# Kernel optimization log

Measured on AMD Instinct MI355X. Metric: run time of the kernel, lower is better.

## Reference

```python
import jax, jax.numpy as jnp
import numpy as np

CHUNK = 64
EPS = 1e-5


def segsum(a):
    # a: (..., T) -> (..., T, T) lower-triangular cumulative segment sums; -inf above diag
    T = a.shape[-1]
    cs = jnp.cumsum(a, axis=-1)
    ss = cs[..., :, None] - cs[..., None, :]
    mask = jnp.tril(jnp.ones((T, T), dtype=bool))
    return jnp.where(mask, ss, -jnp.inf)


def ssd(x, A, B, C, chunk):
    # x: (b, L, h, p), A: (b, L, h), B/C: (b, L, n)
    b, L, h, p = x.shape
    c = L // chunk
    x = x.reshape(b, c, chunk, h, p)
    A = A.reshape(b, c, chunk, h).transpose(0, 3, 1, 2)          # b h c l
    B = B.reshape(b, c, chunk, -1)                               # b c l n
    C = C.reshape(b, c, chunk, -1)                               # b c l n
    A_cum = jnp.cumsum(A, axis=-1)                               # b h c l
    Lmat = jnp.exp(segsum(A))                                    # b h c l l (causal decay)
    # intra-chunk (diagonal-block) output
    Y_diag = jnp.einsum('bcln,bcsn,bhcls,bcshp->bclhp', C, B, Lmat, x)
    # per-chunk states
    decay_states = jnp.exp(A_cum[..., -1:] - A_cum)              # b h c l
    states = jnp.einsum('bcln,bhcl,bclhp->bchpn', B, decay_states, x)
    states = jnp.concatenate([jnp.zeros_like(states[:, :1]), states], axis=1)  # b (c+1) h p n
    # inter-chunk recurrence via chunk-level segsum
    A_last = jnp.pad(A_cum[..., -1], ((0, 0), (0, 0), (1, 0)))   # b h (c+1)
    decay_chunk = jnp.exp(segsum(A_last))                        # b h (c+1) (c+1)
    new_states = jnp.einsum('bhzc,bchpn->bzhpn', decay_chunk, states)
    states, final = new_states[:, :-1], new_states[:, -1:]
    Y_off = jnp.einsum('bcln,bchpn,bhcl->bclhp', C, states, jnp.exp(A_cum))
    return (Y_diag + Y_off).reshape(b, L, h, p), final


def mamba2(x, W_in, conv_w, conv_b, dt_bias, A_log, D, norm_w, W_out):
    d_inner = norm_w.shape[0]
    nheads = dt_bias.shape[0]
    d_state = (conv_b.shape[0] - d_inner) // 2
    headdim = d_inner // nheads
    k_conv = conv_w.shape[0]
    b, L, _ = x.shape

    zxbcdt = x @ W_in                                            # (b, L, 2*d_inner+2*n+h)
    z = zxbcdt[..., :d_inner]
    xBC = zxbcdt[..., d_inner:2 * d_inner + 2 * d_state]
    dt = jax.nn.softplus(zxbcdt[..., 2 * d_inner + 2 * d_state:] + dt_bias)  # (b, L, h)
    A = -jnp.exp(A_log)                                          # (h,)

    # causal depthwise conv (zero init conv state == left-pad k_conv-1 zeros) + silu
    xp = jnp.pad(xBC, ((0, 0), (k_conv - 1, 0), (0, 0)))
    xBC = jax.lax.conv_general_dilated(
        xp, conv_w, (1,), 'VALID',
        dimension_numbers=('NWC', 'WIO', 'NWC'),
        feature_group_count=conv_b.shape[0])
    xBC = jax.nn.silu(xBC + conv_b)

    xs = xBC[..., :d_inner].reshape(b, L, nheads, headdim)       # (b, L, h, p)
    Bm = xBC[..., d_inner:d_inner + d_state]                     # (b, L, n)
    Cm = xBC[..., d_inner + d_state:]                            # (b, L, n)

    Y, _ = ssd(xs * dt[..., None], A * dt, Bm, Cm, CHUNK)
    Y = Y + xs * D                                               # D: (h, 1) broadcasts over p
    y = Y.reshape(b, L, d_inner)

    # gated RMSNorm
    y = y * jax.nn.silu(z)
    y = y * jax.lax.rsqrt(jnp.mean(y * y, axis=-1, keepdims=True) + EPS) * norm_w
    return y @ W_out


def setup_inputs():
    key = jax.random.key(0)
    ks = jax.random.split(key, 8)
    B, L, d_model = 2, 4096, 1024
    expand, d_state, k_conv, headdim = 2, 128, 4, 64
    d_inner = expand * d_model
    nheads = d_inner // headdim
    d_in_proj = 2 * d_inner + 2 * d_state + nheads
    conv_dim = d_inner + 2 * d_state
    return {
        'x': jax.random.normal(ks[0], (B, L, d_model), jnp.float32),
        'W_in': jax.random.normal(ks[1], (d_model, d_in_proj), jnp.float32) / np.sqrt(d_model).astype(np.float32),
        'conv_w': jax.random.normal(ks[2], (k_conv, 1, conv_dim), jnp.float32) / np.sqrt(k_conv).astype(np.float32),
        'conv_b': jnp.zeros((conv_dim,), jnp.float32),
        'dt_bias': jax.random.normal(ks[3], (nheads,), jnp.float32) * 0.5 - 2.0,
        'A_log': jnp.log(1.0 + 15.0 * jax.random.uniform(ks[4], (nheads,), jnp.float32)),
        'D': jax.random.normal(ks[5], (nheads, 1), jnp.float32),
        'norm_w': jnp.ones((d_inner,), jnp.float32),
        'W_out': jax.random.normal(ks[6], (d_inner, d_model), jnp.float32) / np.sqrt(d_inner).astype(np.float32),
    }


def reference(x, W_in, conv_w, conv_b, dt_bias, A_log, D, norm_w, W_out):
    return mamba2(x, W_in, conv_w, conv_b, dt_bias, A_log, D, norm_w, W_out)
```

## Files before the change

### kernel.cpp

```cpp
#include <hip/hip_runtime.h>
#include <hip/hip_fp16.h>

typedef _Float16 f16;
typedef _Float16 f16x4 __attribute__((ext_vector_type(4)));
typedef _Float16 f16x8 __attribute__((ext_vector_type(8)));
typedef float f32x4 __attribute__((ext_vector_type(4)));

#define DEV __device__ __forceinline__

constexpr int BB    = 2;
constexpr int LL    = 4096;
constexpr int DM    = 1024;
constexpr int DIN   = 2048;
constexpr int DST   = 128;
constexpr int NH    = 32;
constexpr int HD    = 64;
constexpr int NC    = 64;
constexpr int MROWS = BB * LL;
constexpr int NPROJ = 2*DIN + 2*DST + NH;
constexpr int NZ    = 2*DIN + 2*DST;
constexpr int CONVD = DIN + 2*DST;
constexpr int DT_OFF = 2*DIN + 2*DST;
constexpr int BOFF  = DIN;
constexpr int COFF  = DIN + DST;

DEV float silu_f(float v) { return v / (1.f + __expf(-v)); }

DEV void gload_lds16(const f16* gsrc, f16* lds_dst) {
  __builtin_amdgcn_global_load_lds(
      (const __attribute__((address_space(1))) void*)gsrc,
      (__attribute__((address_space(3))) void*)lds_dst, 16, 0, 0);
}

__global__ __launch_bounds__(256)
void tof16_kernel(const float* __restrict__ src, f16* __restrict__ dst, int n8) {
  int i = blockIdx.x * 256 + threadIdx.x;
  if (i >= n8) return;
  f32x4 a = *(const f32x4*)(src + (size_t)i*8);
  f32x4 b = *(const f32x4*)(src + (size_t)i*8 + 4);
  f16x8 o;
#pragma unroll
  for (int j = 0; j < 4; ++j) { o[j] = (f16)a[j]; o[4+j] = (f16)b[j]; }
  *(f16x8*)(dst + (size_t)i*8) = o;
}

__global__ __launch_bounds__(256)
void transpose_f32_to_f16(const float* __restrict__ src, f16* __restrict__ dst,
                          int K, int N, int srcLd, const float* __restrict__ colScale) {
  __shared__ float tbuf[32][33];
  int n0 = blockIdx.x * 32, k0 = blockIdx.y * 32;
  int tx = threadIdx.x & 31, ty = threadIdx.x >> 5;
  for (int i = ty; i < 32; i += 8)
    tbuf[i][tx] = src[(size_t)(k0 + i)*srcLd + n0 + tx];
  __syncthreads();
  float cs = colScale ? colScale[k0 + tx] : 1.f;
  for (int i = ty; i < 32; i += 8)
    dst[(size_t)(n0 + i)*K + (k0 + tx)] = (f16)(tbuf[tx][i] * cs);
}

template<int BM, int BN, int WM_, int WN_, bool C16>
__global__ __launch_bounds__(WM_*WN_*64, 2)
void gemm_t(const f16* __restrict__ A, const f16* __restrict__ Bt,
            void* __restrict__ Cp, int M, int N, int K, int ldc,
            const float* __restrict__ rowScale) {
  constexpr int THREADS = WM_*WN_*64;
  constexpr int WTM = BM/WM_, WTN = BN/WN_;
  constexpr int FM = WTM/16, FN = WTN/16;
  constexpr int LA = BM*4/THREADS, LB = BN*4/THREADS;
  __shared__ f16 As[2][BM*32];
  __shared__ f16 Bs[2][BN*32];
  const int nbn = N / BN;
  const int nwg = (int)gridDim.x;
  const int lb  = ((int)blockIdx.x & 7) * (nwg >> 3) + ((int)blockIdx.x >> 3);
  const int bm = lb / nbn, bn = lb % nbn;
  const int tid = threadIdx.x;
  const int wave = tid >> 6, lane = tid & 63;
  const int lrow = lane & 15, kgrp = lane >> 4;
  const int wm = wave / WN_, wn = wave % WN_;
  const int nt = K >> 5;
  const int bcol8 = (kgrp ^ ((lrow ^ (lrow >> 2)) & 3)) * 8;

  const f16* aptr[LA];
  const f16* bptr[LB];
#pragma unroll
  for (int i = 0; i < LA; ++i) {
    int s = tid + i*THREADS, row = s >> 2;
    int g = (s & 3) ^ ((row ^ (row >> 2)) & 3);
    aptr[i] = A + (size_t)(bm*BM + row)*K + g*8;
  }
#pragma unroll
  for (int i = 0; i < LB; ++i) {
    int s = tid + i*THREADS, row = s >> 2;
    int g = (s & 3) ^ ((row ^ (row >> 2)) & 3);
    bptr[i] = Bt + (size_t)(bn*BN + row)*K + g*8;
  }

  f32x4 acc[FM][FN] = {};

  auto STAGE = [&](int buf, int t) {
#pragma unroll
    for (int i = 0; i < LA; ++i)
      gload_lds16(aptr[i] + (size_t)t*32, As[buf] + (wave*64 + i*THREADS)*8);
#pragma unroll
    for (int i = 0; i < LB; ++i)
      gload_lds16(bptr[i] + (size_t)t*32, Bs[buf] + (wave*64 + i*THREADS)*8);
  };

  STAGE(0, 0);
  asm volatile("s_waitcnt vmcnt(0)" ::: "memory");
  __builtin_amdgcn_s_barrier();
  __builtin_amdgcn_sched_barrier(0);

  for (int t = 0; t < nt; ++t) {
    const int cur = t & 1;
    if (t + 1 < nt) STAGE(cur ^ 1, t + 1);
    const f16* Ab = As[cur];
    const f16* Bb = Bs[cur];
    f16x8 bf[FN];
#pragma unroll
    for (int n = 0; n < FN; ++n)
      bf[n] = *(const f16x8*)(Bb + (wn*WTN + n*16 + lrow)*32 + bcol8);
#pragma unroll
    for (int m = 0; m < FM; ++m) {
      f16x8 af = *(const f16x8*)(Ab + (wm*WTM + m*16 + lrow)*32 + bcol8);
#pragma unroll
      for (int n = 0; n < FN; ++n)
        acc[m][n] = __builtin_amdgcn_mfma_f32_16x16x32_f16(af, bf[n], acc[m][n], 0, 0, 0);
    }
    if (t + 1 < nt) {
      asm volatile("s_waitcnt vmcnt(0)" ::: "memory");
      __builtin_amdgcn_s_barrier();
      __builtin_amdgcn_sched_barrier(0);
    }
  }

  int crow0 = bm*BM + wm*WTM, ccol0 = bn*BN + wn*WTN;
#pragma unroll
  for (int m = 0; m < FM; ++m)
#pragma unroll
    for (int n = 0; n < FN; ++n) {
      int r0 = crow0 + m*16 + (lane >> 4)*4;
      int c0 = ccol0 + n*16 + (lane & 15);
#pragma unroll
      for (int r = 0; r < 4; ++r) {
        float v = acc[m][n][r];
        if (rowScale) v *= rowScale[r0 + r];
        if constexpr (C16) {
          f16* C = (f16*)Cp;
          C[(size_t)(r0 + r)*ldc + c0] = (f16)v;
        } else {
          float* C = (float*)Cp;
          C[(size_t)(r0 + r)*ldc + c0] = v;
        }
      }
    }
}

__global__ __launch_bounds__(256)
void dt_kernel(const float* __restrict__ x, const float* __restrict__ Win,
               const float* __restrict__ dt_bias, const float* __restrict__ A_log,
               float* __restrict__ dt, float* __restrict__ Acum) {
  __shared__ float xs[64][132];
  __shared__ float ws[128][32];
  __shared__ float dts[64][32];
  int bc = blockIdx.x;
  int r0 = bc * 64;
  int t = threadIdx.x;
  int r = t >> 2, c0 = (t & 3) * 8;
  float acc[8] = {};
  for (int kt = 0; kt < 1024; kt += 128) {
    __syncthreads();
#pragma unroll
    for (int i = 0; i < 8; ++i) {
      int idx4 = t + i*256;
      int rr = idx4 >> 5, c4 = (idx4 & 31) * 4;
      *(f32x4*)&xs[rr][c4] = *(const f32x4*)(x + (size_t)(r0 + rr)*1024 + kt + c4);
    }
#pragma unroll
    for (int i = 0; i < 4; ++i) {
      int idx4 = t + i*256;
      int rr = idx4 >> 3, c4 = (idx4 & 7) * 4;
      *(f32x4*)&ws[rr][c4] = *(const f32x4*)(Win + (size_t)(kt + rr)*NPROJ + DT_OFF + c4);
    }
    __syncthreads();
#pragma unroll 8
    for (int k = 0; k < 128; ++k) {
      float xv = xs[r][k];
      f32x4 w0 = *(const f32x4*)&ws[k][c0];
      f32x4 w1 = *(const f32x4*)&ws[k][c0 + 4];
#pragma unroll
      for (int j = 0; j < 4; ++j) { acc[j] += xv * w0[j]; acc[4+j] += xv * w1[j]; }
    }
  }
#pragma unroll
  for (int j = 0; j < 8; ++j) {
    float v = acc[j] + dt_bias[c0 + j];
    float sp = (v > 20.f) ? v : log1pf(__expf(v));
    dt[(size_t)(r0 + r)*NH + c0 + j] = sp;
    dts[r][c0 + j] = sp;
  }
  __syncthreads();
  int wave = t >> 6, lane = t & 63;
  for (int hh = 0; hh < 8; ++hh) {
    int h = wave*8 + hh;
    float A = -__expf(A_log[h]);
    float v = A * dts[lane][h];
#pragma unroll
    for (int off = 1; off < 64; off <<= 1) {
      float u = __shfl_up(v, off);
      if (lane >= off) v += u;
    }
    Acum[((size_t)bc*NH + h)*64 + lane] = v;
  }
}

__global__ __launch_bounds__(256)
void conv_kernel(const f16* __restrict__ zxh, const float* __restrict__ cw,
                 const float* __restrict__ cb, f16* __restrict__ out) {
  int i = blockIdx.x * 256 + threadIdx.x;
  int row = i / (CONVD/8);
  int c8  = (i - row*(CONVD/8)) * 8;
  int lb = row & (LL - 1);
  f32x4 a0 = *(const f32x4*)(cb + c8);
  f32x4 a1 = *(const f32x4*)(cb + c8 + 4);
#pragma unroll
  for (int j = 0; j < 4; ++j) {
    int lsrc = lb - 3 + j;
    if (lsrc >= 0) {
      f16x8 v = *(const f16x8*)(zxh + (size_t)(row - 3 + j)*NZ + BOFF + c8);
      f32x4 w0 = *(const f32x4*)(cw + j*CONVD + c8);
      f32x4 w1 = *(const f32x4*)(cw + j*CONVD + c8 + 4);
#pragma unroll
      for (int jj = 0; jj < 4; ++jj) {
        a0[jj] += (float)v[jj]   * w0[jj];
        a1[jj] += (float)v[4+jj] * w1[jj];
      }
    }
  }
  f16x8 o;
#pragma unroll
  for (int jj = 0; jj < 4; ++jj) {
    o[jj]   = (f16)silu_f(a0[jj]);
    o[4+jj] = (f16)silu_f(a1[jj]);
  }
  *(f16x8*)(out + (size_t)row*CONVD + c8) = o;
}

__global__ __launch_bounds__(256)
void gbuf_kernel(const f16* __restrict__ xbc, f16* __restrict__ G) {
  __shared__ float Cs[64][128];
  __shared__ float Bsm[64][128];
  int bc = blockIdx.x;
  int row0 = bc * 64;
  int t = threadIdx.x;
#pragma unroll
  for (int i = 0; i < 4; ++i) {
    int idx = t + i*256;
    int r = idx >> 4, c8 = (idx & 15) * 8;
    f16x8 cv = *(const f16x8*)(xbc + (size_t)(row0 + r)*CONVD + COFF + c8);
    f16x8 bv = *(const f16x8*)(xbc + (size_t)(row0 + r)*CONVD + BOFF + c8);
    f32x4 c0v = {(float)cv[0], (float)cv[1], (float)cv[2], (float)cv[3]};
    f32x4 c1v = {(float)cv[4], (float)cv[5], (float)cv[6], (float)cv[7]};
    f32x4 b0v = {(float)bv[0], (float)bv[1], (float)bv[2], (float)bv[3]};
    f32x4 b1v = {(float)bv[4], (float)bv[5], (float)bv[6], (float)bv[7]};
    *(f32x4*)&Cs[r][c8]      = c0v;  *(f32x4*)&Cs[r][c8 + 4]  = c1v;
    *(f32x4*)&Bsm[r][c8]     = b0v;  *(f32x4*)&Bsm[r][c8 + 4] = b1v;
  }
  __syncthreads();
  int l0 = (t >> 4)*4, s0 = (t & 15)*4;
  float acc[4][4] = {};
  for (int n4 = 0; n4 < 128; n4 += 4) {
    f32x4 cv[4], bv[4];
#pragma unroll
    for (int i = 0; i < 4; ++i) cv[i] = *(const f32x4*)&Cs[l0 + i][n4];
#pragma unroll
    for (int j = 0; j < 4; ++j) bv[j] = *(const f32x4*)&Bsm[s0 + j][n4];
#pragma unroll
    for (int i = 0; i < 4; ++i)
#pragma unroll
      for (int j = 0; j < 4; ++j)
        acc[i][j] += cv[i][0]*bv[j][0] + cv[i][1]*bv[j][1] + cv[i][2]*bv[j][2] + cv[i][3]*bv[j][3];
  }
#pragma unroll
  for (int i = 0; i < 4; ++i) {
    f16x4 v = {(f16)acc[i][0], (f16)acc[i][1], (f16)acc[i][2], (f16)acc[i][3]};
    *(f16x4*)(G + ((size_t)bc*64 + l0 + i)*64 + s0) = v;
  }
}

__global__ __launch_bounds__(256)
void ssd_states_kernel(const f16* __restrict__ xbc, const float* __restrict__ dtb,
                       const float* __restrict__ Acum, f16* __restrict__ states) {
  __shared__ union {
    struct { f16 XdT[64][72]; f16 BT[128][72]; } s;
    float Sl[64][132];
  } u;
  __shared__ float ac[64], dts[64];
  int bc = blockIdx.x >> 5, h = blockIdx.x & 31;
  int row0 = bc*64, t = threadIdx.x;
  if (t < 64) {
    ac[t]  = Acum[((size_t)bc*NH + h)*64 + t];
    dts[t] = dtb[(size_t)(row0 + t)*NH + h];
  }
  __syncthreads();
  float ac63 = ac[63];
#pragma unroll
  for (int i = 0; i < 2; ++i) {
    int idx = t + i*256; int l = idx >> 3, p8 = (idx & 7)*8;
    f16x8 v = *(const f16x8*)(xbc + (size_t)(row0 + l)*CONVD + h*HD + p8);
    float d = dts[l];
#pragma unroll
    for (int j = 0; j < 8; ++j) u.s.XdT[p8 + j][l] = (f16)((float)v[j]*d);
  }
#pragma unroll
  for (int i = 0; i < 4; ++i) {
    int idx = t + i*256; int l = idx >> 4, n8 = (idx & 15)*8;
    f16x8 v = *(const f16x8*)(xbc + (size_t)(row0 + l)*CONVD + BOFF + n8);
    float dl = __expf(ac63 - ac[l]);
#pragma unroll
    for (int j = 0; j < 8; ++j) u.s.BT[n8 + j][l] = (f16)((float)v[j]*dl);
  }
  __syncthreads();
  int wave = t >> 6, lane = t & 63;
  int lrow = lane & 15, kgrp = lane >> 4;
  f32x4 sacc[8] = {};
#pragma unroll
  for (int kk = 0; kk < 64; kk += 32) {
    f16x8 afs = *(const f16x8*)&u.s.XdT[wave*16 + lrow][kk + kgrp*8];
#pragma unroll
    for (int n = 0; n < 8; ++n) {
      f16x8 bf = *(const f16x8*)&u.s.BT[n*16 + lrow][kk + kgrp*8];
      sacc[n] = __builtin_amdgcn_mfma_f32_16x16x32_f16(afs, bf, sacc[n], 0, 0, 0);
    }
  }
  __syncthreads();
#pragma unroll
  for (int n = 0; n < 8; ++n)
#pragma unroll
    for (int r = 0; r < 4; ++r)
      u.Sl[wave*16 + kgrp*4 + r][n*16 + lrow] = sacc[n][r];
  __syncthreads();
  size_t sb = ((size_t)bc*NH + h)*8192;
#pragma unroll
  for (int i = 0; i < 4; ++i) {
    int idx = t + i*256; int p = idx >> 4, n8 = (idx & 15)*8;
    f16x8 o;
#pragma unroll
    for (int j = 0; j < 8; ++j) o[j] = (f16)u.Sl[p][n8 + j];
    *(f16x8*)(states + sb + (size_t)p*128 + n8) = o;
  }
}

__global__ __launch_bounds__(256)
void scan_kernel(f16* __restrict__ states, const float* __restrict__ Acum) {
  int bid = blockIdx.x;
  int bh = bid >> 3, pgrp = bid & 7;
  int b = bh >> 5, h = bh & 31;
  int t = threadIdx.x;
  int p = pgrp*8 + (t >> 5), n4 = (t & 31) * 4;
  size_t off = (size_t)p*128 + n4;
  f32x4 carry = {0.f, 0.f, 0.f, 0.f};
  for (int c = 0; c < NC; ++c) {
    size_t base = ((size_t)(b*NC + c)*NH + h)*8192;
    f16x4 cv = *(f16x4*)(states + base + off);
    f16x4 st;
#pragma unroll
    for (int j = 0; j < 4; ++j) st[j] = (f16)carry[j];
    *(f16x4*)(states + base + off) = st;
    float tc = __expf(Acum[((size_t)(b*NC + c)*NH + h)*64 + 63]);
#pragma unroll
    for (int j = 0; j < 4; ++j) carry[j] = carry[j]*tc + (float)cv[j];
  }
}

__global__ __launch_bounds__(256)
void yoff_kernel(const f16* __restrict__ xbc, const f16* __restrict__ zxh,
                 const f16* __restrict__ Gg, const f16* __restrict__ states,
                 const float* __restrict__ dtb, const float* __restrict__ Acum,
                 const float* __restrict__ Dp, f16* __restrict__ Ybuf) {
  __shared__ union {
    struct { f16 Gt[64][72]; f16 XdT[64][72]; } a;
    struct { f16 Ch[64][136]; f16 Sin[64][136]; } b;
    float Yl2[64][68];
  } u;
  __shared__ float Yl[64][68];
  __shared__ float ac[64], dts[64], eac[64];
  int bc = blockIdx.x >> 5, h = blockIdx.x & 31;
  int row0 = bc*64, t = threadIdx.x;
  if (t < 64) {
    float a0 = Acum[((size_t)bc*NH + h)*64 + t];
    ac[t]  = a0;
    eac[t] = __expf(a0);
    dts[t] = dtb[(size_t)(row0 + t)*NH + h];
  }
  __syncthreads();
#pragma unroll
  for (int i = 0; i < 2; ++i) {
    int idx = t + i*256; int l = idx >> 3, p8 = (idx & 7)*8;
    f16x8 v = *(const f16x8*)(xbc + (size_t)(row0 + l)*CONVD + h*HD + p8);
    float d = dts[l];
#pragma unroll
    for (int j = 0; j < 8; ++j) u.a.XdT[p8 + j][l] = (f16)((float)v[j]*d);
  }
#pragma unroll
  for (int i = 0; i < 2; ++i) {
    int idx = t + i*256; int l = idx >> 3, s8 = (idx & 7)*8;
    f16x8 g = *(const f16x8*)(Gg + (size_t)bc*4096 + l*64 + s8);
    float al = ac[l];
    f16x8 o;
#pragma unroll
    for (int j = 0; j < 8; ++j) {
      int s = s8 + j;
      o[j] = (l >= s) ? (f16)((float)g[j] * __expf(al - ac[s])) : (f16)0.f;
    }
    *(f16x8*)&u.a.Gt[l][s8] = o;
  }
  __syncthreads();
  int wave = t >> 6, lane = t & 63;
  int lrow = lane & 15, kgrp = lane >> 4;
  f32x4 yacc[4] = {};
#pragma unroll
  for (int kk = 0; kk < 64; kk += 32) {
    f16x8 afy = *(const f16x8*)&u.a.Gt[wave*16 + lrow][kk + kgrp*8];
#pragma unroll
    for (int n = 0; n < 4; ++n) {
      f16x8 bf = *(const f16x8*)&u.a.XdT[n*16 + lrow][kk + kgrp*8];
      yacc[n] = __builtin_amdgcn_mfma_f32_16x16x32_f16(afy, bf, yacc[n], 0, 0, 0);
    }
  }
  __syncthreads();
#pragma unroll
  for (int n = 0; n < 4; ++n)
#pragma unroll
    for (int r = 0; r < 4; ++r)
      Yl[wave*16 + kgrp*4 + r][n*16 + lrow] = yacc[n][r];
  size_t sb = ((size_t)bc*NH + h)*8192;
#pragma unroll
  for (int i = 0; i < 4; ++i) {
    int idx = t + i*256; int r = idx >> 4, c8 = (idx & 15)*8;
    *(f16x8*)&u.b.Ch[r][c8]  = *(const f16x8*)(xbc + (size_t)(row0 + r)*CONVD + COFF + c8);
    *(f16x8*)&u.b.Sin[r][c8] = *(const f16x8*)(states + sb + (size_t)r*128 + c8);
  }
  __syncthreads();
  f32x4 acc[4] = {};
#pragma unroll
  for (int kk = 0; kk < 128; kk += 32) {
    f16x8 af = *(const f16x8*)&u.b.Ch[wave*16 + lrow][kk + kgrp*8];
#pragma unroll
    for (int n = 0; n < 4; ++n) {
      f16x8 bf = *(const f16x8*)&u.b.Sin[n*16 + lrow][kk + kgrp*8];
      acc[n] = __builtin_amdgcn_mfma_f32_16x16x32_f16(af, bf, acc[n], 0, 0, 0);
    }
  }
  __syncthreads();
#pragma unroll
  for (int n = 0; n < 4; ++n)
#pragma unroll
    for (int r = 0; r < 4; ++r)
      u.Yl2[wave*16 + kgrp*4 + r][n*16 + lrow] = acc[n][r];
  __syncthreads();
  float Dh = Dp[h];
#pragma unroll
  for (int i = 0; i < 2; ++i) {
    int idx = t + i*256; int l = idx >> 3, p8 = (idx & 7)*8;
    int row = row0 + l;
    f16x8 zh = *(const f16x8*)(zxh + (size_t)row*NZ + h*HD + p8);
    f16x8 xs = *(const f16x8*)(xbc + (size_t)row*CONVD + h*HD + p8);
    float e = eac[l];
    f16x8 o;
#pragma unroll
    for (int j = 0; j < 8; ++j) {
      float yv = Yl[l][p8 + j] + e*u.Yl2[l][p8 + j] + (float)xs[j]*Dh;
      o[j] = (f16)(yv * silu_f((float)zh[j]));
    }
    *(f16x8*)(Ybuf + (size_t)row*DIN + h*HD + p8) = o;
  }
}

__global__ __launch_bounds__(256)
void rms_scale_kernel(const f16* __restrict__ yg, float* __restrict__ scale) {
  __shared__ float red[4];
  int row = blockIdx.x, t = threadIdx.x;
  f16x8 v = *(const f16x8*)(yg + (size_t)row*DIN + t*8);
  float ss = 0.f;
#pragma unroll
  for (int j = 0; j < 8; ++j) { float f = (float)v[j]; ss += f*f; }
#pragma unroll
  for (int off = 32; off > 0; off >>= 1) ss += __shfl_down(ss, off);
  if ((t & 63) == 0) red[t >> 6] = ss;
  __syncthreads();
  if (t == 0) {
    float tot = red[0] + red[1] + red[2] + red[3];
    scale[row] = rsqrtf(tot * (1.f/2048.f) + 1e-5f);
  }
}

extern "C" void kernel_launch(void* const* d_in, const int* in_sizes, int n_in,
                              void* d_out, int out_size, void* d_ws, size_t ws_size,
                              hipStream_t stream) {
  const float* x       = (const float*)d_in[0];
  const float* W_in    = (const float*)d_in[1];
  const float* conv_w  = (const float*)d_in[2];
  const float* conv_b  = (const float*)d_in[3];
  const float* dt_bias = (const float*)d_in[4];
  const float* A_log   = (const float*)d_in[5];
  const float* Dp      = (const float*)d_in[6];
  const float* norm_w  = (const float*)d_in[7];
  const float* W_out   = (const float*)d_in[8];

  constexpr size_t WS_NEED = 213909504;
  if (ws_size < WS_NEED) return;

  char* w = (char*)d_ws;
  f16*   states = (f16*)(w + 0);
  f16*   winT   = (f16*)(w + 0);
  f16*   xh     = (f16*)(w + 33554432);
  f16*   woutT  = (f16*)(w + 33554432);
  f16*   zxh    = (f16*)(w + 67108864);
  f16*   xbcc   = (f16*)(w + 138412032);
  f16*   Ybuf   = (f16*)(w + 176160768);
  float* dtb    = (float*)(w + 209715200);
  float* Acum   = (float*)(w + 210763776);
  f16*   Gg     = (f16*)(w + 211812352);
  float* rscale = (float*)(w + 212860928);

  tof16_kernel<<<4096, 256, 0, stream>>>(x, xh, MROWS*DM/8);
  transpose_f32_to_f16<<<dim3(NZ/32, DM/32), 256, 0, stream>>>(W_in, winT, DM, NZ, NPROJ, nullptr);
  gemm_t<256,128,4,2,true><<<(MROWS/256)*(NZ/128), 512, 0, stream>>>(xh, winT, zxh, MROWS, NZ, DM, NZ, nullptr);
  dt_kernel<<<MROWS/64, 256, 0, stream>>>(x, W_in, dt_bias, A_log, dtb, Acum);
  conv_kernel<<<MROWS*(CONVD/8)/256, 256, 0, stream>>>(zxh, conv_w, conv_b, xbcc);
  gbuf_kernel<<<BB*NC, 256, 0, stream>>>(xbcc, Gg);
  ssd_states_kernel<<<BB*NC*NH, 256, 0, stream>>>(xbcc, dtb, Acum, states);
  scan_kernel<<<BB*NH*8, 256, 0, stream>>>(states, Acum);
  yoff_kernel<<<BB*NC*NH, 256, 0, stream>>>(xbcc, zxh, Gg, states, dtb, Acum, Dp, Ybuf);
  transpose_f32_to_f16<<<dim3(DM/32, DIN/32), 256, 0, stream>>>(W_out, woutT, DIN, DM, DM, norm_w);
  rms_scale_kernel<<<MROWS, 256, 0, stream>>>(Ybuf, rscale);
  gemm_t<128,128,2,2,false><<<(MROWS/128)*(DM/128), 256, 0, stream>>>(Ybuf, woutT, d_out, MROWS, DM, DIN, DM, rscale);
}
```

Measured before the change: 426.0 us.

## Fuse x fp16 conversion into dt kernel; reuse B tile across four heads

Removes the standalone fp32-to-fp16 conversion kernel. dt_kernel, which already reads x, now writes the fp16 copy, and it is launched before the input GEMM. ssd_states_kernel now processes four heads per block: it loads the shared B tile once and moves the decay factor onto the x side, which cuts redundant B loads and exp work. The cost is fewer blocks (a quarter as many), a serial loop over heads inside each block, and larger LDS use now that the union is gone.

```diff
diff --git a/kernel.cpp b/kernel.cpp
--- a/kernel.cpp
+++ b/kernel.cpp
@@ -30,18 +30,6 @@
   __builtin_amdgcn_global_load_lds(
       (const __attribute__((address_space(1))) void*)gsrc,
       (__attribute__((address_space(3))) void*)lds_dst, 16, 0, 0);
-}
-
-__global__ __launch_bounds__(256)
-void tof16_kernel(const float* __restrict__ src, f16* __restrict__ dst, int n8) {
-  int i = blockIdx.x * 256 + threadIdx.x;
-  if (i >= n8) return;
-  f32x4 a = *(const f32x4*)(src + (size_t)i*8);
-  f32x4 b = *(const f32x4*)(src + (size_t)i*8 + 4);
-  f16x8 o;
-#pragma unroll
-  for (int j = 0; j < 4; ++j) { o[j] = (f16)a[j]; o[4+j] = (f16)b[j]; }
-  *(f16x8*)(dst + (size_t)i*8) = o;
 }
 
 __global__ __launch_bounds__(256)
@@ -159,7 +147,8 @@
 __global__ __launch_bounds__(256)
 void dt_kernel(const float* __restrict__ x, const float* __restrict__ Win,
                const float* __restrict__ dt_bias, const float* __restrict__ A_log,
-               float* __restrict__ dt, float* __restrict__ Acum) {
+               float* __restrict__ dt, float* __restrict__ Acum,
+               f16* __restrict__ xh) {
   __shared__ float xs[64][132];
   __shared__ float ws[128][32];
   __shared__ float dts[64][32];
@@ -174,7 +163,10 @@
     for (int i = 0; i < 8; ++i) {
       int idx4 = t + i*256;
       int rr = idx4 >> 5, c4 = (idx4 & 31) * 4;
-      *(f32x4*)&xs[rr][c4] = *(const f32x4*)(x + (size_t)(r0 + rr)*1024 + kt + c4);
+      f32x4 xv4 = *(const f32x4*)(x + (size_t)(r0 + rr)*1024 + kt + c4);
+      *(f32x4*)&xs[rr][c4] = xv4;
+      f16x4 xo = {(f16)xv4[0], (f16)xv4[1], (f16)xv4[2], (f16)xv4[3]};
+      *(f16x4*)(xh + (size_t)(r0 + rr)*1024 + kt + c4) = xo;
     }
 #pragma unroll
     for (int i = 0; i < 4; ++i) {
@@ -291,63 +283,65 @@
 __global__ __launch_bounds__(256)
 void ssd_states_kernel(const f16* __restrict__ xbc, const float* __restrict__ dtb,
                        const float* __restrict__ Acum, f16* __restrict__ states) {
-  __shared__ union {
-    struct { f16 XdT[64][72]; f16 BT[128][72]; } s;
-    float Sl[64][132];
-  } u;
+  __shared__ f16 BT[128][72];
+  __shared__ f16 XdT[64][72];
+  __shared__ float Sl[64][132];
   __shared__ float ac[64], dts[64];
-  int bc = blockIdx.x >> 5, h = blockIdx.x & 31;
+  int bc = blockIdx.x >> 3, hg = blockIdx.x & 7;
   int row0 = bc*64, t = threadIdx.x;
-  if (t < 64) {
-    ac[t]  = Acum[((size_t)bc*NH + h)*64 + t];
-    dts[t] = dtb[(size_t)(row0 + t)*NH + h];
-  }
-  __syncthreads();
-  float ac63 = ac[63];
-#pragma unroll
-  for (int i = 0; i < 2; ++i) {
-    int idx = t + i*256; int l = idx >> 3, p8 = (idx & 7)*8;
-    f16x8 v = *(const f16x8*)(xbc + (size_t)(row0 + l)*CONVD + h*HD + p8);
-    float d = dts[l];
-#pragma unroll
-    for (int j = 0; j < 8; ++j) u.s.XdT[p8 + j][l] = (f16)((float)v[j]*d);
-  }
+  int wave = t >> 6, lane = t & 63;
+  int lrow = lane & 15, kgrp = lane >> 4;
 #pragma unroll
   for (int i = 0; i < 4; ++i) {
     int idx = t + i*256; int l = idx >> 4, n8 = (idx & 15)*8;
     f16x8 v = *(const f16x8*)(xbc + (size_t)(row0 + l)*CONVD + BOFF + n8);
-    float dl = __expf(ac63 - ac[l]);
-#pragma unroll
-    for (int j = 0; j < 8; ++j) u.s.BT[n8 + j][l] = (f16)((float)v[j]*dl);
-  }
-  __syncthreads();
-  int wave = t >> 6, lane = t & 63;
-  int lrow = lane & 15, kgrp = lane >> 4;
-  f32x4 sacc[8] = {};
-#pragma unroll
-  for (int kk = 0; kk < 64; kk += 32) {
-    f16x8 afs = *(const f16x8*)&u.s.XdT[wave*16 + lrow][kk + kgrp*8];
-#pragma unroll
-    for (int n = 0; n < 8; ++n) {
-      f16x8 bf = *(const f16x8*)&u.s.BT[n*16 + lrow][kk + kgrp*8];
-      sacc[n] = __builtin_amdgcn_mfma_f32_16x16x32_f16(afs, bf, sacc[n], 0, 0, 0);
-    }
-  }
-  __syncthreads();
-#pragma unroll
-  for (int n = 0; n < 8; ++n)
-#pragma unroll
-    for (int r = 0; r < 4; ++r)
-      u.Sl[wave*16 + kgrp*4 + r][n*16 + lrow] = sacc[n][r];
-  __syncthreads();
-  size_t sb = ((size_t)bc*NH + h)*8192;
-#pragma unroll
-  for (int i = 0; i < 4; ++i) {
-    int idx = t + i*256; int p = idx >> 4, n8 = (idx & 15)*8;
-    f16x8 o;
-#pragma unroll
-    for (int j = 0; j < 8; ++j) o[j] = (f16)u.Sl[p][n8 + j];
-    *(f16x8*)(states + sb + (size_t)p*128 + n8) = o;
+#pragma unroll
+    for (int j = 0; j < 8; ++j) BT[n8 + j][l] = v[j];
+  }
+  for (int hh = 0; hh < 4; ++hh) {
+    int h = hg*4 + hh;
+    __syncthreads();
+    if (t < 64) {
+      ac[t]  = Acum[((size_t)bc*NH + h)*64 + t];
+      dts[t] = dtb[(size_t)(row0 + t)*NH + h];
+    }
+    __syncthreads();
+    float ac63 = ac[63];
+#pragma unroll
+    for (int i = 0; i < 2; ++i) {
+      int idx = t + i*256; int l = idx >> 3, p8 = (idx & 7)*8;
+      f16x8 v = *(const f16x8*)(xbc + (size_t)(row0 + l)*CONVD + h*HD + p8);
+      float d = dts[l] * __expf(ac63 - ac[l]);
+#pragma unroll
+      for (int j = 0; j < 8; ++j) XdT[p8 + j][l] = (f16)((float)v[j]*d);
+    }
+    __syncthreads();
+    f32x4 sacc[8] = {};
+#pragma unroll
+    for (int kk = 0; kk < 64; kk += 32) {
+      f16x8 afs = *(const f16x8*)&XdT[wave*16 + lrow][kk + kgrp*8];
+#pragma unroll
+      for (int n = 0; n < 8; ++n) {
+        f16x8 bf = *(const f16x8*)&BT[n*16 + lrow][kk + kgrp*8];
+        sacc[n] = __builtin_amdgcn_mfma_f32_16x16x32_f16(afs, bf, sacc[n], 0, 0, 0);
+      }
+    }
+    __syncthreads();
+#pragma unroll
+    for (int n = 0; n < 8; ++n)
+#pragma unroll
+      for (int r = 0; r < 4; ++r)
+        Sl[wave*16 + kgrp*4 + r][n*16 + lrow] = sacc[n][r];
+    __syncthreads();
+    size_t sb = ((size_t)bc*NH + h)*8192;
+#pragma unroll
+    for (int i = 0; i < 4; ++i) {
+      int idx = t + i*256; int p = idx >> 4, n8 = (idx & 15)*8;
+      f16x8 o;
+#pragma unroll
+      for (int j = 0; j < 8; ++j) o[j] = (f16)Sl[p][n8 + j];
+      *(f16x8*)(states + sb + (size_t)p*128 + n8) = o;
+    }
   }
 }
 
@@ -524,13 +518,12 @@
   f16*   Gg     = (f16*)(w + 211812352);
   float* rscale = (float*)(w + 212860928);
 
-  tof16_kernel<<<4096, 256, 0, stream>>>(x, xh, MROWS*DM/8);
+  dt_kernel<<<MROWS/64, 256, 0, stream>>>(x, W_in, dt_bias, A_log, dtb, Acum, xh);
   transpose_f32_to_f16<<<dim3(NZ/32, DM/32), 256, 0, stream>>>(W_in, winT, DM, NZ, NPROJ, nullptr);
   gemm_t<256,128,4,2,true><<<(MROWS/256)*(NZ/128), 512, 0, stream>>>(xh, winT, zxh, MROWS, NZ, DM, NZ, nullptr);
-  dt_kernel<<<MROWS/64, 256, 0, stream>>>(x, W_in, dt_bias, A_log, dtb, Acum);
   conv_kernel<<<MROWS*(CONVD/8)/256, 256, 0, stream>>>(zxh, conv_w, conv_b, xbcc);
   gbuf_kernel<<<BB*NC, 256, 0, stream>>>(xbcc, Gg);
-  ssd_states_kernel<<<BB*NC*NH, 256, 0, stream>>>(xbcc, dtb, Acum, states);
+  ssd_states_kernel<<<BB*NC*(NH/4), 256, 0, stream>>>(xbcc, dtb, Acum, states);
   scan_kernel<<<BB*NH*8, 256, 0, stream>>>(states, Acum);
   yoff_kernel<<<BB*NC*NH, 256, 0, stream>>>(xbcc, zxh, Gg, states, dtb, Acum, Dp, Ybuf);
   transpose_f32_to_f16<<<dim3(DM/32, DIN/32), 256, 0, stream>>>(W_out, woutT, DIN, DM, DM, norm_w);
```

After: 392.6 us. 1.09x faster.
